# Kernel tuning notes

Hardware: AMD Instinct MI355X
Metric: run time of the kernel (lower is better)

## Reference

```python
import jax, jax.numpy as jnp
import numpy as np

B, S, D, H = 1, 1024, 1024, 16
DR, DV, R = 64, 64, 256          # rope head dim, v head dim, kv_lora_rank (qk_nope_head_dim = 0)
V, L, E, F, TOPK = 32000, 2, 4, 4096, 2
EPS, THETA, LB_WEIGHT = 1e-6, 10000.0, 0.01
SCALE = DR ** -0.5               # q_head_dim = nope(0) + rope(64)


def rms_norm(x, w):
    return x * jax.lax.rsqrt(jnp.mean(x * x, axis=-1, keepdims=True) + EPS) * w


def rotate_half(x):
    h = x.shape[-1] // 2
    return jnp.concatenate([-x[..., h:], x[..., :h]], axis=-1)


def apply_rope(x, cos, sin):
    # DeepSeek-V3 rotary: interleaved->half reorder, then rotate-half
    *lead, d = x.shape
    x = x.reshape(*lead, d // 2, 2).swapaxes(-1, -2).reshape(*lead, d)
    return x * cos + rotate_half(x) * sin


def setup_inputs() -> dict:
    key = jax.random.key(0)
    ks = iter(jax.random.split(key, 40))
    w = lambda shape: (0.02 * jax.random.normal(next(ks), shape)).astype(jnp.float32)
    return dict(
        tokens=jax.random.randint(next(ks), (B, S), 0, V, dtype=jnp.int32),
        embed=w((V, D)),                      # tied embedding / lm_head
        q_w=w((L, H * DR, D)),                # q_proj (q_lora_rank=None)
        kva_w=w((L, R + DR, D)),              # kv_a_proj_with_mqa
        kva_ln=jnp.ones((L, R), jnp.float32), # kv_a_layernorm (RMSNorm)
        kvb_w=w((L, H * DV, R)),              # kv_b_proj (nope=0 -> values only)
        o_w=w((L, D, H * DV)),
        norm1_w=jnp.ones((L, D), jnp.float32),
        norm2_w=jnp.ones((L, D), jnp.float32),
        router_w=w((L, E, D)),
        router_b=jnp.zeros((L, E), jnp.float32),
        w1=w((L, E, D, F)),
        b1=jnp.zeros((L, E, F), jnp.float32),
        w2=w((L, E, F, D)),
        b2=jnp.zeros((L, E, D), jnp.float32),
        final_norm_w=jnp.ones((D,), jnp.float32),
    )


def _layer(x, p, cos, sin, mask):
    # --- MLHA attention (DeepSeek-V3, qk_nope=0 => keys are shared rope k_pe) ---
    h = rms_norm(x, p['norm1_w'])
    q = (h @ p['q_w'].T).reshape(B, S, H, DR).transpose(0, 2, 1, 3)        # [B,H,S,DR]
    kva = h @ p['kva_w'].T                                                 # [B,S,R+DR]
    ckv, k_pe = kva[..., :R], kva[..., R:]
    v = (rms_norm(ckv, p['kva_ln']) @ p['kvb_w'].T).reshape(B, S, H, DV).transpose(0, 2, 1, 3)
    q = apply_rope(q, cos[None, None], sin[None, None])
    k = apply_rope(k_pe[:, None], cos[None, None], sin[None, None])[:, 0]  # [B,S,DR] shared across heads
    scores = jnp.einsum('bhsd,btd->bhst', q, k) * SCALE + mask
    attn = jax.nn.softmax(scores, axis=-1)
    o = jnp.einsum('bhst,bhtd->bhsd', attn, v).transpose(0, 2, 1, 3).reshape(B, S, H * DV)
    x = x + o @ p['o_w'].T
    # --- MoE FFN (top-k routing, renormalized gates, switch-style aux loss) ---
    h2 = rms_norm(x, p['norm2_w']).reshape(B * S, D)
    probs = jax.nn.softmax(h2 @ p['router_w'].T + p['router_b'], axis=-1)  # [T,E]
    topv, topi = jax.lax.top_k(probs, TOPK)
    gates = topv / jnp.sum(topv, axis=-1, keepdims=True)
    sel = jax.nn.one_hot(topi, E, dtype=probs.dtype)                       # [T,K,E]
    combine = jnp.einsum('tke,tk->te', sel, gates)                         # [T,E]
    hmid = jax.nn.gelu(jnp.einsum('td,edf->tef', h2, p['w1']) + p['b1'], approximate=False)
    y = jnp.einsum('tef,efd->ted', hmid, p['w2']) + p['b2']                # [T,E,D]
    ff = jnp.einsum('te,ted->td', combine, y).reshape(B, S, D)
    frac = jnp.mean(jnp.max(sel, axis=1), axis=0)                          # token fraction per expert
    aux = E * jnp.sum(frac * jnp.mean(probs, axis=0))
    return x + ff, aux


def reference(tokens, embed, q_w, kva_w, kva_ln, kvb_w, o_w, norm1_w, norm2_w,
              router_w, router_b, w1, b1, w2, b2, final_norm_w):
    x = embed[tokens]                                                      # [B,S,D]
    inv = 1.0 / (THETA ** (jnp.arange(0, DR, 2, dtype=jnp.float32) / DR))
    freqs = jnp.arange(S, dtype=jnp.float32)[:, None] * inv[None, :]
    emb = jnp.concatenate([freqs, freqs], axis=-1)
    cos, sin = jnp.cos(emb), jnp.sin(emb)                                  # [S,DR]
    mask = jnp.where(jnp.triu(jnp.ones((S, S), bool), 1), -jnp.inf, 0.0)[None, None]
    stacked = dict(q_w=q_w, kva_w=kva_w, kva_ln=kva_ln, kvb_w=kvb_w, o_w=o_w,
                   norm1_w=norm1_w, norm2_w=norm2_w, router_w=router_w, router_b=router_b,
                   w1=w1, b1=b1, w2=w2, b2=b2)

    def step(carry, p):
        x, aux = carry
        x, a = _layer(x, p, cos, sin, mask)
        return (x, aux + a), None

    (x, aux), _ = jax.lax.scan(step, (x, jnp.float32(0.0)), stacked)
    x = rms_norm(x, final_norm_w)
    logits = x @ embed.T                                                   # tied lm_head
    return logits, aux * LB_WEIGHT
```

## Files before the change

### kernel.cpp

```cpp
#include <hip/hip_runtime.h>
#include <hip/hip_bf16.h>
#include <math.h>

typedef __hip_bfloat16 bf16;
typedef __attribute__((ext_vector_type(8))) short short8;
typedef __attribute__((ext_vector_type(4))) short short4v;
typedef __attribute__((ext_vector_type(4))) float f32x4;

static constexpr int SEQ  = 1024;
static constexpr int DIM  = 1024;
static constexpr int NH   = 16;
static constexpr int DRR  = 64;
static constexpr int RR   = 256;
static constexpr int KVAN = RR + DRR;
static constexpr int VOC  = 32000;
static constexpr int NEXP = 4;
static constexpr int FFD  = 4096;
static constexpr int NSLOT = SEQ*2;
static constexpr float EPSF = 1e-6f;
static constexpr float ATT_SCALE = 0.125f;
static constexpr float LBW = 0.01f;

__device__ __forceinline__ bool is_bf(const uint32_t* mg){ return *mg == 0x3F803F80u; }
__device__ __forceinline__ float ldin(const void* p, size_t i, bool bf){
// ... 189 lines not shown
}

__global__ __launch_bounds__(256) void k_gather2(const float* __restrict__ h2,
    const int* __restrict__ tos, short* __restrict__ S){
  const int slot = blockIdx.x, tid = threadIdx.x;
  const int t = tos[slot];
  const int i = tid*4;
  const float4 v = *(const float4*)&h2[(size_t)t*DIM + i];
  const float vv[4] = {v.x, v.y, v.z, v.w};
  short4v h, l;
  #pragma unroll
  for (int q = 0; q < 4; ++q){ short a,b; split2(vv[q], a, b); h[q]=a; l[q]=b; }
  *(short4v*)&S[(size_t)slot*2*DIM + i] = h;
  *(short4v*)&S[(size_t)slot*2*DIM + DIM + i] = l;
}

__device__ __forceinline__ void tg_stage(const short* __restrict__ A, int lda, int ac,
    const short* __restrict__ B, int ldb, int bc, int bm, int bn,
    short* sA, short* sB, int wid, int rA, int ss){
  #pragma unroll
  for (int j = 0; j < 4; ++j){
    const int row = wid*32 + j*8 + rA;
    gload16(A + (size_t)(bm+row)*lda + ac + ss*8, sA + (wid*32 + j*8)*64);
    gload16(B + (size_t)(bn+row)*ldb + bc + ss*8, sB + (wid*32 + j*8)*64);
  }
}

#define TG_MFMAS(sAp, sBp)                                                      \
    _Pragma("unroll")                                                           \
    for (int kk = 0; kk < 2; ++kk){                                             \
      short8 a[4], b[4];                                                        \
      _Pragma("unroll")                                                         \
      for (int f = 0; f < 4; ++f){                                              \
        const int ar = wr*64 + f*16 + lr;                                       \
        a[f] = *(const short8*)&(sAp)[ar*64 + (((kk*4+lks)^(ar&7)))*8];         \
        const int br = wc*64 + f*16 + lr;                                       \
        b[f] = *(const short8*)&(sBp)[br*64 + (((kk*4+lks)^(br&7)))*8];         \
      }                                                                         \
      _Pragma("unroll")                                                         \
      for (int f = 0; f < 4; ++f)                                               \
        _Pragma("unroll")                                                       \
        for (int g = 0; g < 4; ++g)                                             \
          acc[f*4+g] = __builtin_amdgcn_mfma_f32_16x16x32_bf16(                 \
              a[f], b[g], acc[f*4+g], 0, 0, 0);                                 \
    }

#define TG_KADDR(st)                                                            \
  const int kt = (st)*64;                                                       \
  const int t = (kt >= 2*K) ? 2 : (kt >= K) ? 1 : 0;                            \
  const int ko = kt - t*K;                                                      \
  const int ac = ko + ((t == 2) ? K : 0);                                       \
  const int bc = ko + ((t == 1) ? K : 0);

template<int MODE>
__global__ __launch_bounds__(256) void k_tgemm_wt(
    const short* __restrict__ A, int lda,
    const short* __restrict__ W, int ldb, int K, int nt,
    float* __restrict__ C, int N, int S, float* __restrict__ Cpart){
  __shared__ alignas(16) short sA[128*64];
  __shared__ alignas(16) short sB[128*64];
  const int tid = threadIdx.x;
  const int wid = tid >> 6, lane = tid & 63;
  const int wr = wid >> 1, wc = wid & 1;
  const int bm = blockIdx.y * 128, bn = blockIdx.x * 128;
  const int rA = lane >> 3, ss = (lane & 7) ^ rA;
  const int lr = lane & 15, lks = lane >> 4;
  f32x4 acc[16];
  #pragma unroll
  for (int i = 0; i < 16; ++i) acc[i] = f32x4{0,0,0,0};

  const int nsteps = (nt*K) >> 6;
  const int per = (nsteps + S - 1)/S;
  const int st0 = blockIdx.z*per, st1 = min(nsteps, st0 + per);
  for (int st = st0; st < st1; ++st){
    TG_KADDR(st)
    tg_stage(A, lda, ac, W, ldb, bc, bm, bn, sA, sB, wid, rA, ss);
    __syncthreads();
    TG_MFMAS(sA, sB)
    __syncthreads();
  }
  const int r4 = lks*4, cj = lr;
  if (S == 1){
    #pragma unroll
    for (int f = 0; f < 4; ++f)
      #pragma unroll
      for (int g = 0; g < 4; ++g)
        #pragma unroll
        for (int r = 0; r < 4; ++r){
          const int gm = bm + wr*64 + f*16 + r4 + r;
          const int gn = bn + wc*64 + g*16 + cj;
          if (gn >= N) continue;
          const size_t idx = (size_t)gm*N + gn;
          if (MODE == 0) C[idx] = acc[f*4+g][r];
          else           C[idx] += acc[f*4+g][r];
        }
  } else {
    const int M = gridDim.y * 128;
    float* P = Cpart + (size_t)blockIdx.z*M*N;
    #pragma unroll
    for (int f = 0; f < 4; ++f)
      #pragma unroll
      for (int g = 0; g < 4; ++g)
        #pragma unroll
        for (int r = 0; r < 4; ++r){
          const int gm = bm + wr*64 + f*16 + r4 + r;
          const int gn = bn + wc*64 + g*16 + cj;
          if (gn >= N) continue;
          P[(size_t)gm*N + gn] = acc[f*4+g][r];
        }
  }
}

__global__ __launch_bounds__(512, 2) void k_tgemm_wtL(
    const short* __restrict__ A, int lda,
    const short* __restrict__ W, int ldb, int K,
    float* __restrict__ C, int N){
  __shared__ alignas(16) short sA[2][256*64];
  __shared__ alignas(16) short sB[2][256*64];
  const int tid = threadIdx.x;
  const int wid = tid >> 6, lane = tid & 63;
  const int wr = wid >> 2, wc = wid & 3;
  const int T = gridDim.x * gridDim.y;
  const int p = blockIdx.x + gridDim.x * blockIdx.y;
  const int xcd = p & 7, idx = p >> 3;
  const int q = T >> 3, r = T & 7;
  const int u = ((xcd < r) ? xcd*(q+1) : r*(q+1) + (xcd-r)*q) + idx;
  const int bn = (u >> 2) * 256;
  const int bm = (u & 3) * 256;
  const int rA = lane >> 3, ss = (lane & 7) ^ rA;
  const int lr = lane & 15, lks = lane >> 4;
  f32x4 acc[32];
  #pragma unroll
  for (int i = 0; i < 32; ++i) acc[i] = f32x4{0,0,0,0};

  auto stage = [&](int ko, int buf){
    #pragma unroll
    for (int j = 0; j < 4; ++j){
      const int row = wid*32 + j*8 + rA;
      gload16(A + (size_t)(bm+row)*lda + ko + ss*8, sA[buf] + (wid*32 + j*8)*64);
      gload16(W + (size_t)(bn+row)*ldb + ko + ss*8, sB[buf] + (wid*32 + j*8)*64);
    }
  };

  const int nsteps = K >> 6;
  stage(0, 0);
  asm volatile("s_waitcnt vmcnt(0)" ::: "memory");
  __builtin_amdgcn_s_barrier();
  int cur = 0;
  for (int st = 0; st < nsteps; ++st){
    const bool pf = (st + 1 < nsteps);
    if (pf) stage((st + 1)*64, cur^1);
    __builtin_amdgcn_s_setprio(1);
    #pragma unroll
    for (int kk = 0; kk < 2; ++kk){
      short8 a[8], b[4];
      #pragma unroll
      for (int f = 0; f < 8; ++f){
        const int ar = wr*128 + f*16 + lr;
        a[f] = *(const short8*)&sA[cur][ar*64 + (((kk*4+lks)^(ar&7)))*8];
      }
      #pragma unroll
      for (int g = 0; g < 4; ++g){
        const int br = wc*64 + g*16 + lr;
        b[g] = *(const short8*)&sB[cur][br*64 + (((kk*4+lks)^(br&7)))*8];
      }
      #pragma unroll
      for (int f = 0; f < 8; ++f)
        #pragma unroll
        for (int g = 0; g < 4; ++g)
          acc[f*4+g] = __builtin_amdgcn_mfma_f32_16x16x32_bf16(
              a[f], b[g], acc[f*4+g], 0, 0, 0);
    }
    __builtin_amdgcn_s_setprio(0);
    if (pf){
      asm volatile("s_waitcnt vmcnt(0)" ::: "memory");
      __builtin_amdgcn_s_barrier();
      cur ^= 1;
    }
  }
  const int r4 = lks*4, cj = lr;
  #pragma unroll
  for (int f = 0; f < 8; ++f)
    #pragma unroll
    for (int g = 0; g < 4; ++g)
      #pragma unroll
      for (int rr = 0; rr < 4; ++rr){
        const int gm = bm + wr*128 + f*16 + r4 + rr;
        const int gn = bn + wc*64 + g*16 + cj;
        if (gn >= N) continue;
        C[(size_t)gm*N + gn] = acc[f*4+g][rr];
      }
}

template<int MODE>
__global__ __launch_bounds__(256) void k_redw(const float* __restrict__ Cpart,
    float* __restrict__ C, int total, int S){
  const int i = blockIdx.x*256 + threadIdx.x;
  if (i >= total) return;
  float v = 0.f;
  for (int s = 0; s < S; ++s) v += Cpart[(size_t)s*total + i];
  if (MODE == 0) C[i] = v;
  else           C[i] += v;
}

template<int ACT, int OSPLIT>
__global__ __launch_bounds__(256) void k_tgemm_grp(
    const short* __restrict__ A, int lda,
    const short* __restrict__ Wall, int ldb, int K, int nt,
    const void* __restrict__ bias, size_t biofs, size_t perexp_bias,
    float* __restrict__ Cf, short* __restrict__ Cs,
    const int* __restrict__ meta, int N, const uint32_t* mg,
    int S, float* __restrict__ Cpart){
  __shared__ alignas(16) short sA[2][128*64];
  __shared__ alignas(16) short sB[2][128*64];
  const bool bf = is_bf(mg);
  const int e = blockIdx.z / S, zs = blockIdx.z - e*S;
  const int cnt = meta[e], off = meta[NEXP + e];
  const int r0 = blockIdx.y * 128;
  if (r0 >= cnt) return;
  const int rows_valid = min(128, cnt - r0);
  const int bm = off + r0, bn = blockIdx.x * 128;
  const short* W = Wall + (size_t)e*(size_t)N*ldb;
  const size_t bib = biofs + (size_t)e * perexp_bias;

  const int tid = threadIdx.x;
  const int wid = tid >> 6, lane = tid & 63;
  const int wr = wid >> 1, wc = wid & 1;
  const int rA = lane >> 3, ss = (lane & 7) ^ rA;
  const int lr = lane & 15, lks = lane >> 4;
  f32x4 acc[16];
  #pragma unroll
  for (int i = 0; i < 16; ++i) acc[i] = f32x4{0,0,0,0};

  const int nsteps = (nt*K) >> 6;
  const int per = (nsteps + S - 1)/S;
  const int st0 = zs*per, st1 = min(nsteps, st0 + per);
  {
    TG_KADDR(st0)
    tg_stage(A, lda, ac, W, ldb, bc, bm, bn, sA[0], sB[0], wid, rA, ss);
    asm volatile("s_waitcnt vmcnt(0)" ::: "memory");
    __builtin_amdgcn_s_barrier();
  }
  int cur = 0;
  for (int st = st0; st < st1; ++st){
    const bool pf = (st + 1 < st1);
    if (pf){
      TG_KADDR(st+1)
      tg_stage(A, lda, ac, W, ldb, bc, bm, bn, sA[cur^1], sB[cur^1], wid, rA, ss);
    }
    __builtin_amdgcn_s_setprio(1);
    TG_MFMAS(sA[cur], sB[cur])
    __builtin_amdgcn_s_setprio(0);
    if (pf){
      asm volatile("s_waitcnt vmcnt(0)" ::: "memory");
      __builtin_amdgcn_s_barrier();
      cur ^= 1;
    }
  }
  const int r4 = lks*4, cj = lr;
  if (S == 1){
    #pragma unroll
    for (int f = 0; f < 4; ++f)
      #pragma unroll
      for (int g = 0; g < 4; ++g)
        #pragma unroll
        for (int r = 0; r < 4; ++r){
          const int rin = wr*64 + f*16 + r4 + r;
          if (rin >= rows_valid) continue;
          const int gn = bn + wc*64 + g*16 + cj;
          float v = acc[f*4+g][r] + ldin(bias, bib + gn, bf);
          if (ACT == 1) v = 0.5f * v * (1.f + erff(v * 0.70710678118654752f));
          if (OSPLIT){
            short hi, lo; split2(v, hi, lo);
            const size_t idx = (size_t)(bm + rin)*2*N + gn;
            Cs[idx] = hi; Cs[idx + N] = lo;
          } else {
            Cf[(size_t)(bm + rin)*N + gn] = v;
          }
        }
  } else {
    float* P = Cpart + (size_t)zs*NSLOT*N;
    #pragma unroll
    for (int f = 0; f < 4; ++f)
      #pragma unroll
      for (int g = 0; g < 4; ++g)
        #pragma unroll
        for (int r = 0; r < 4; ++r){
          const int rin = wr*64 + f*16 + r4 + r;
          if (rin >= rows_valid) continue;
          const int gn = bn + wc*64 + g*16 + cj;
          P[(size_t)(bm + rin)*N + gn] = acc[f*4+g][r];
        }
  }
}

template<int ACT, int OSPLIT>
__global__ __launch_bounds__(512, 2) void k_tgemm_grpF(
    const short* __restrict__ A, int lda,
    const short* __restrict__ Wall, int ldb, int K,
    const void* __restrict__ bias, size_t biofs, size_t perexp_bias,
    float* __restrict__ Cf, short* __restrict__ Cs,
    const int* __restrict__ meta, int N, const uint32_t* mg,
    int S, float* __restrict__ Cpart){
  __shared__ alignas(16) short sAh[256*64];
  __shared__ alignas(16) short sAl[256*64];
  __shared__ alignas(16) short sBh[256*64];
  __shared__ alignas(16) short sBl[256*64];
  const bool bf = is_bf(mg);
  const int e = blockIdx.z / S, zs = blockIdx.z - e*S;
  const int cnt = meta[e], off = meta[NEXP + e];
  const int r0 = blockIdx.y * 256;
  if (r0 >= cnt) return;
  const int rows_valid = min(256, cnt - r0);
  const int bm = off + r0, bn = blockIdx.x * 256;
  const short* W = Wall + (size_t)e*(size_t)N*ldb;
  const size_t bib = biofs + (size_t)e * perexp_bias;

  const int tid = threadIdx.x;
  const int wid = tid >> 6, lane = tid & 63;
  const int wr = wid >> 2, wc = wid & 3;
  const int rA = lane >> 3, ss = (lane & 7) ^ rA;
  const int lr = lane & 15, lks = lane >> 4;
  f32x4 acc[32];
  #pragma unroll
  for (int i = 0; i < 32; ++i) acc[i] = f32x4{0,0,0,0};

  const int nsteps = K >> 6;
  const int per = (nsteps + S - 1)/S;
  const int st0 = zs*per, st1 = min(nsteps, st0 + per);
  for (int st = st0; st < st1; ++st){
    const int ko = st*64;
    #pragma unroll
    for (int j = 0; j < 4; ++j){
      const int row = wid*32 + j*8 + rA;
      const size_t arow = (size_t)(bm+row)*lda;
      const size_t brow = (size_t)(bn+row)*ldb;
      const int dst = (wid*32 + j*8)*64;
      gload16(A + arow + ko + ss*8,     sAh + dst);
      gload16(A + arow + K + ko + ss*8, sAl + dst);
      gload16(W + brow + ko + ss*8,     sBh + dst);
      gload16(W + brow + K + ko + ss*8, sBl + dst);
    }
    __syncthreads();
    __builtin_amdgcn_s_setprio(1);
    #pragma unroll
    for (int kk = 0; kk < 2; ++kk){
      short8 bh[4], bl[4];
      #pragma unroll
      for (int g = 0; g < 4; ++g){
        const int br = wc*64 + g*16 + lr;
        const int bo = br*64 + (((kk*4+lks)^(br&7)))*8;
        bh[g] = *(const short8*)&sBh[bo];
        bl[g] = *(const short8*)&sBl[bo];
      }
      #pragma unroll
      for (int f = 0; f < 8; ++f){
        const int ar = wr*128 + f*16 + lr;
        const int ao = ar*64 + (((kk*4+lks)^(ar&7)))*8;
        const short8 ah = *(const short8*)&sAh[ao];
        const short8 al = *(const short8*)&sAl[ao];
        #pragma unroll
        for (int g = 0; g < 4; ++g){
          acc[f*4+g] = __builtin_amdgcn_mfma_f32_16x16x32_bf16(ah, bh[g], acc[f*4+g], 0, 0, 0);
          acc[f*4+g] = __builtin_amdgcn_mfma_f32_16x16x32_bf16(ah, bl[g], acc[f*4+g], 0, 0, 0);
          acc[f*4+g] = __builtin_amdgcn_mfma_f32_16x16x32_bf16(al, bh[g], acc[f*4+g], 0, 0, 0);
        }
      }
    }
    __builtin_amdgcn_s_setprio(0);
    __syncthreads();
  }
  const int r4 = lks*4, cj = lr;
  if (S == 1){
    #pragma unroll
    for (int f = 0; f < 8; ++f)
      #pragma unroll
      for (int g = 0; g < 4; ++g)
        #pragma unroll
        for (int r = 0; r < 4; ++r){
          const int rin = wr*128 + f*16 + r4 + r;
          if (rin >= rows_valid) continue;
          const int gn = bn + wc*64 + g*16 + cj;
          float v = acc[f*4+g][r] + ldin(bias, bib + gn, bf);
          if (ACT == 1) v = 0.5f * v * (1.f + erff(v * 0.70710678118654752f));
          if (OSPLIT){
            short hi, lo; split2(v, hi, lo);
            const size_t idx = (size_t)(bm + rin)*2*N + gn;
            Cs[idx] = hi; Cs[idx + N] = lo;
          } else {
            Cf[(size_t)(bm + rin)*N + gn] = v;
          }
        }
  } else {
    float* P = Cpart + (size_t)zs*NSLOT*N;
    #pragma unroll
    for (int f = 0; f < 8; ++f)
      #pragma unroll
      for (int g = 0; g < 4; ++g)
        #pragma unroll
        for (int r = 0; r < 4; ++r){
          const int rin = wr*128 + f*16 + r4 + r;
          if (rin >= rows_valid) continue;
          const int gn = bn + wc*64 + g*16 + cj;
          P[(size_t)(bm + rin)*N + gn] = acc[f*4+g][r];
        }
  }
}

template<int ACT, int OSPLIT>
__global__ __launch_bounds__(256) void k_redg(const float* __restrict__ Cpart, int S,
    const int* __restrict__ eid,
    const void* __restrict__ bias, size_t biofs, size_t perexp_bias,
    float* __restrict__ Cf, short* __restrict__ Cs, int N, const uint32_t* mg){
  const bool bf = is_bf(mg);
  const int slot = blockIdx.x;
  const int e = eid[slot];
  const size_t bib = biofs + (size_t)e * perexp_bias;
  for (int n = threadIdx.x; n < N; n += 256){
    float v = 0.f;
    for (int s = 0; s < S; ++s)
      v += Cpart[(size_t)s*NSLOT*N + (size_t)slot*N + n];
    v += ldin(bias, bib + n, bf);
    if (ACT == 1) v = 0.5f * v * (1.f + erff(v * 0.70710678118654752f));
    if (OSPLIT){
      short hi, lo; split2(v, hi, lo);
      const size_t idx = (size_t)slot*2*N + n;
      Cs[idx] = hi; Cs[idx + N] = lo;
    } else {
      Cf[(size_t)slot*N + n] = v;
    }
  }
}

__global__ __launch_bounds__(512) void k_ropeq2(const float* __restrict__ qraw,
    const float* __restrict__ cosb, const float* __restrict__ sinb,
    short* __restrict__ Qsp){
  const int t = blockIdx.x, tid = threadIdx.x;
  const int hh = tid >> 5, i = tid & 31;
  const size_t base = (size_t)t*DIM + hh*DRR;
  const float u0 = qraw[base + 2*i];
  const float u1 = qraw[base + 2*i + 1];
  const float c = cosb[t*32 + i], s = sinb[t*32 + i];
  const float o0 = u0*c - u1*s;
  const float o1 = u1*c + u0*s;
  short h0,l0,h1,l1;
  split2(o0,h0,l0); split2(o1,h1,l1);
  short* q = Qsp + ((size_t)hh*SEQ + t)*128;
  q[i] = h0;      q[64+i] = l0;
  q[i+32] = h1;   q[96+i] = l1;
}

__global__ void k_ropek2(const float* __restrict__ kva,
    const float* __restrict__ cosb, const float* __restrict__ sinb,
    short* __restrict__ Kb){
  const int t = blockIdx.x, i = threadIdx.x;
  const float u0 = kva[(size_t)t*KVAN + RR + 2*i];
  const float u1 = kva[(size_t)t*KVAN + RR + 2*i + 1];
  const float c = cosb[t*32 + i], s = sinb[t*32 + i];
  const float o0 = u0*c - u1*s;
  const float o1 = u1*c + u0*s;
  short h0,l0,h1,l1;
  split2(o0,h0,l0); split2(o1,h1,l1);
  short* k = Kb + (size_t)t*128;
  k[i] = h0;      k[64+i] = l0;
  k[i+32] = h1;   k[96+i] = l1;
}

__global__ __launch_bounds__(256) void k_vsplit(const float* __restrict__ vbuf,
    short* __restrict__ Vt){
  __shared__ float tbuf[32][33];
  const int kv0 = blockIdx.x*32, d0 = blockIdx.y*32;
  const int c = threadIdx.x & 31, rb = threadIdx.x >> 5;
  #pragma unroll
  for (int p = 0; p < 4; ++p){
    const int r = rb + p*8;
    tbuf[r][c] = vbuf[(size_t)(kv0 + r)*DIM + d0 + c];
  }
  __syncthreads();
  #pragma unroll
  for (int p = 0; p < 4; ++p){
    const int rr = rb + p*8;
    const int dg = d0 + rr;
    const int h = dg >> 6, dl = dg & 63;
    short hi, lo; split2(tbuf[c][rr], hi, lo);
    const size_t o = ((size_t)h*64 + dl)*2048 + kv0 + c;
    Vt[o] = hi; Vt[o + 1024] = lo;
  }
}

__global__ __launch_bounds__(256) void k_fattn(
    const short* __restrict__ Qsp, const short* __restrict__ Kb,
    const short* __restrict__ Vt, float* __restrict__ outb){
  __shared__ alignas(16) short Qsh[64*64], Qsl[64*64];
  __shared__ alignas(16) short Ksh[64*64], Ksl[64*64];
  __shared__ alignas(16) short Vsh[64*64], Vsl[64*64];
  __shared__ alignas(16) short Ph[64*64], Pl[64*64];
  const int qt = blockIdx.x, hh = blockIdx.y;
  const int qbase = qt*64;
  const int tid = threadIdx.x;
  const int w = tid >> 6, lane = tid & 63;
  const int lr = lane & 15, lks = lane >> 4;
  const int r4 = lks*4, cj = lr;

  stage64(Qsp + ((size_t)hh*SEQ + qbase)*128,      128, Qsh, w, lane);
  stage64(Qsp + ((size_t)hh*SEQ + qbase)*128 + 64, 128, Qsl, w, lane);

  float m_r[4], l_r[4], alpha[4], rmax[4], rsum[4];
  f32x4 o[4];
  #pragma unroll
  for (int r = 0; r < 4; ++r){ m_r[r] = -3.0e38f; l_r[r] = 0.f; }
  #pragma unroll
  for (int g = 0; g < 4; ++g) o[g] = f32x4{0,0,0,0};
  __syncthreads();

  for (int kt = 0; kt <= qt; ++kt){
    const int kvbase = kt*64;
    stage64(Kb + (size_t)kvbase*128,        128, Ksh, w, lane);
    stage64(Kb + (size_t)kvbase*128 + 64,   128, Ksl, w, lane);
    stage64(Vt + (size_t)hh*64*2048 + kvbase,        2048, Vsh, w, lane);
    stage64(Vt + (size_t)hh*64*2048 + 1024 + kvbase, 2048, Vsl, w, lane);
    __syncthreads();

    f32x4 s[4];
    #pragma unroll
    for (int g = 0; g < 4; ++g) s[g] = f32x4{0,0,0,0};
    #pragma unroll
    for (int term = 0; term < 3; ++term){
      const short* Ab = (term == 2) ? Qsl : Qsh;
      const short* Bb = (term == 1) ? Ksl : Ksh;
      #pragma unroll
      for (int ks = 0; ks < 2; ++ks){
        const int arow = w*16 + lr;
        const short8 a = *(const short8*)&Ab[arow*64 + (((ks*4+lks)^(arow&7))*8)];
        #pragma unroll
        for (int g = 0; g < 4; ++g){
          const int brow = g*16 + lr;
          const short8 b = *(const short8*)&Bb[brow*64 + (((ks*4+lks)^(brow&7))*8)];
          s[g] = __builtin_amdgcn_mfma_f32_16x16x32_bf16(a, b, s[g], 0, 0, 0);
        }
      }
    }
    #pragma unroll
    for (int r = 0; r < 4; ++r) rmax[r] = -3.0e38f;
    #pragma unroll
    for (int g = 0; g < 4; ++g)
      #pragma unroll
      for (int r = 0; r < 4; ++r){
        float v = s[g][r] * ATT_SCALE;
        if (kvbase + g*16 + cj > qbase + w*16 + r4 + r) v = -3.0e38f;
        s[g][r] = v;
        rmax[r] = fmaxf(rmax[r], v);
      }
    #pragma unroll
    for (int msk = 1; msk < 16; msk <<= 1)
      #pragma unroll
      for (int r = 0; r < 4; ++r)
        rmax[r] = fmaxf(rmax[r], __shfl_xor(rmax[r], msk));
    #pragma unroll
    for (int r = 0; r < 4; ++r){
      const float mn = fmaxf(m_r[r], rmax[r]);
      alpha[r] = expf(m_r[r] - mn);
      m_r[r] = mn;
      rsum[r] = 0.f;
    }
    #pragma unroll
    for (int g = 0; g < 4; ++g)
      #pragma unroll
      for (int r = 0; r < 4; ++r){
        const float p = expf(s[g][r] - m_r[r]);
        s[g][r] = p;
        rsum[r] += p;
      }
    #pragma unroll
    for (int msk = 1; msk < 16; msk <<= 1)
      #pragma unroll
      for (int r = 0; r < 4; ++r)
        rsum[r] += __shfl_xor(rsum[r], msk);
    #pragma unroll
    for (int r = 0; r < 4; ++r)
      l_r[r] = l_r[r]*alpha[r] + rsum[r];
    #pragma unroll
    for (int g = 0; g < 4; ++g)
      #pragma unroll
      for (int r = 0; r < 4; ++r)
        o[g][r] *= alpha[r];
    #pragma unroll
    for (int g = 0; g < 4; ++g)
      #pragma unroll
      for (int r = 0; r < 4; ++r){
        short hi, lo; split2(s[g][r], hi, lo);
        const int prow = w*16 + r4 + r;
        const int sl = g*2 + (cj >> 3);
        const int addr = prow*64 + ((sl ^ (prow & 7))*8) + (cj & 7);
        Ph[addr] = hi; Pl[addr] = lo;
      }
    #pragma unroll
    for (int term = 0; term < 3; ++term){
      const short* Ab = (term == 2) ? Pl : Ph;
      const short* Bb = (term == 1) ? Vsl : Vsh;
      #pragma unroll
      for (int ks = 0; ks < 2; ++ks){
        const int arow = w*16 + lr;
        const short8 a = *(const short8*)&Ab[arow*64 + (((ks*4+lks)^(arow&7))*8)];
        #pragma unroll
        for (int g = 0; g < 4; ++g){
          const int brow = g*16 + lr;
          const short8 b = *(const short8*)&Bb[brow*64 + (((ks*4+lks)^(brow&7))*8)];
          o[g] = __builtin_amdgcn_mfma_f32_16x16x32_bf16(a, b, o[g], 0, 0, 0);
        }
      }
    }
    __syncthreads();
  }
  #pragma unroll
  for (int g = 0; g < 4; ++g)
    #pragma unroll
    for (int r = 0; r < 4; ++r)
      outb[(size_t)(qbase + w*16 + r4 + r)*DIM + hh*64 + g*16 + cj] = o[g][r] / l_r[r];
}

template<int MODE>
__global__ __launch_bounds__(256) void k_mgemm_wt(const float* __restrict__ A,
    const void* __restrict__ W, size_t wofs, float* __restrict__ C,
    int M, int N, int K, const uint32_t* mg){
  __shared__ alignas(16) short As[64][40];
  __shared__ alignas(16) short Bs[64][40];
  const bool bf = is_bf(mg);
  const int tid = threadIdx.x;
  const int bm = blockIdx.x * 64, bn = blockIdx.y * 64;
  const int wid = tid >> 6, lane = tid & 63;
  const int wr = wid >> 1, wc = wid & 1;
  const int lrow = lane & 15, lk = (lane >> 4) * 8;
  const int srow = tid >> 3, sk = (tid & 7) * 4;
  f32x4 acc00{0,0,0,0}, acc01{0,0,0,0}, acc10{0,0,0,0}, acc11{0,0,0,0};
  for (int kt = 0; kt < K; kt += 32){
    #pragma unroll
    for (int p = 0; p < 2; ++p){
      const int r = srow + p*32;
      const size_t abase = (size_t)(bm + r)*K + kt + sk;
      As[r][sk+0] = f2bs(A[abase+0]);
      As[r][sk+1] = f2bs(A[abase+1]);
      As[r][sk+2] = f2bs(A[abase+2]);
      As[r][sk+3] = f2bs(A[abase+3]);
      const size_t wbase = wofs + (size_t)(bn + r)*K + kt + sk;
      Bs[r][sk+0] = f2bs(ldin(W, wbase+0, bf));
      Bs[r][sk+1] = f2bs(ldin(W, wbase+1, bf));
      Bs[r][sk+2] = f2bs(ldin(W, wbase+2, bf));
      Bs[r][sk+3] = f2bs(ldin(W, wbase+3, bf));
    }
    __syncthreads();
    const short8 a0 = *(const short8*)&As[wr*32 +      lrow][lk];
    const short8 a1 = *(const short8*)&As[wr*32 + 16 + lrow][lk];
    const short8 b0 = *(const short8*)&Bs[wc*32 +      lrow][lk];
    const short8 b1 = *(const short8*)&Bs[wc*32 + 16 + lrow][lk];
    acc00 = __builtin_amdgcn_mfma_f32_16x16x32_bf16(a0, b0, acc00, 0, 0, 0);
    acc01 = __builtin_amdgcn_mfma_f32_16x16x32_bf16(a0, b1, acc01, 0, 0, 0);
    acc10 = __builtin_amdgcn_mfma_f32_16x16x32_bf16(a1, b0, acc10, 0, 0, 0);
    acc11 = __builtin_amdgcn_mfma_f32_16x16x32_bf16(a1, b1, acc11, 0, 0, 0);
    __syncthreads();
  }
  const int r4 = (lane >> 4) * 4, cj = lane & 15;
  #pragma unroll
  for (int fm = 0; fm < 2; ++fm)
    #pragma unroll
    for (int fn = 0; fn < 2; ++fn){
      const f32x4 av = fm == 0 ? (fn == 0 ? acc00 : acc01) : (fn == 0 ? acc10 : acc11);
      #pragma unroll
      for (int r = 0; r < 4; ++r){
        const int gm = bm + wr*32 + fm*16 + r4 + r;
        const int gn = bn + wc*32 + fn*16 + cj;
        const size_t idx = (size_t)gm*N + gn;
        if (MODE == 0) C[idx] = av[r];
        else           C[idx] += av[r];
// ... 399 lines not shown
```

Before: 1.421 ms.

## Double-buffer LDS tiles in grouped expert GEMM with K-step 32 prefetch

The grouped MoE GEMM now splits its LDS tiles into two buffers of half the K depth (32 instead of 64). The next K-slice is prefetched with async global-to-LDS loads while MFMAs run on the current buffer, and one barrier per step replaces two. The aim is to hide global load latency behind compute, at the cost of twice as many loop iterations and barriers per K and a new XOR swizzle over 4 chunks instead of 8.

```diff
diff --git a/kernel.cpp b/kernel.cpp
--- a/kernel.cpp
+++ b/kernel.cpp
@@ -515,10 +515,10 @@
     float* __restrict__ Cf, short* __restrict__ Cs,
     const int* __restrict__ meta, int N, const uint32_t* mg,
     int S, float* __restrict__ Cpart){
-  __shared__ alignas(16) short sAh[256*64];
-  __shared__ alignas(16) short sAl[256*64];
-  __shared__ alignas(16) short sBh[256*64];
-  __shared__ alignas(16) short sBl[256*64];
+  __shared__ alignas(16) short sAh[2][256*32];
+  __shared__ alignas(16) short sAl[2][256*32];
+  __shared__ alignas(16) short sBh[2][256*32];
+  __shared__ alignas(16) short sBl[2][256*32];
   const bool bf = is_bf(mg);
   const int e = blockIdx.z / S, zs = blockIdx.z - e*S;
   const int cnt = meta[e], off = meta[NEXP + e];
@@ -532,46 +532,53 @@
   const int tid = threadIdx.x;
   const int wid = tid >> 6, lane = tid & 63;
   const int wr = wid >> 2, wc = wid & 3;
-  const int rA = lane >> 3, ss = (lane & 7) ^ rA;
+  const int rA4 = lane >> 2, ss4 = (lane & 3) ^ (rA4 & 3);
   const int lr = lane & 15, lks = lane >> 4;
   f32x4 acc[32];
   #pragma unroll
   for (int i = 0; i < 32; ++i) acc[i] = f32x4{0,0,0,0};
 
-  const int nsteps = K >> 6;
+  auto stage = [&](int ko, int buf){
+    #pragma unroll
+    for (int j = 0; j < 2; ++j){
+      const int row = j*128 + wid*16 + rA4;
+      const int dst = (j*128 + wid*16)*32 + lane*8;
+      const size_t arow = (size_t)(bm+row)*lda;
+      const size_t brow = (size_t)(bn+row)*ldb;
+      const int sc = ko + ss4*8;
+      gload16(A + arow + sc,     &sAh[buf][dst]);
+      gload16(A + arow + K + sc, &sAl[buf][dst]);
+      gload16(W + brow + sc,     &sBh[buf][dst]);
+      gload16(W + brow + K + sc, &sBl[buf][dst]);
+    }
+  };
+
+  const int nsteps = K >> 5;
   const int per = (nsteps + S - 1)/S;
   const int st0 = zs*per, st1 = min(nsteps, st0 + per);
+  stage(st0*32, 0);
+  asm volatile("s_waitcnt vmcnt(0)" ::: "memory");
+  __builtin_amdgcn_s_barrier();
+  int cur = 0;
   for (int st = st0; st < st1; ++st){
-    const int ko = st*64;
-    #pragma unroll
-    for (int j = 0; j < 4; ++j){
-      const int row = wid*32 + j*8 + rA;
-      const size_t arow = (size_t)(bm+row)*lda;
-      const size_t brow = (size_t)(bn+row)*ldb;
-      const int dst = (wid*32 + j*8)*64;
-      gload16(A + arow + ko + ss*8,     sAh + dst);
-      gload16(A + arow + K + ko + ss*8, sAl + dst);
-      gload16(W + brow + ko + ss*8,     sBh + dst);
-      gload16(W + brow + K + ko + ss*8, sBl + dst);
-    }
-    __syncthreads();
+    const bool pf = (st + 1 < st1);
+    if (pf) stage((st + 1)*32, cur^1);
     __builtin_amdgcn_s_setprio(1);
-    #pragma unroll
-    for (int kk = 0; kk < 2; ++kk){
+    {
       short8 bh[4], bl[4];
       #pragma unroll
       for (int g = 0; g < 4; ++g){
         const int br = wc*64 + g*16 + lr;
-        const int bo = br*64 + (((kk*4+lks)^(br&7)))*8;
-        bh[g] = *(const short8*)&sBh[bo];
-        bl[g] = *(const short8*)&sBl[bo];
+        const int bo = br*32 + ((lks ^ (br&3))*8);
+        bh[g] = *(const short8*)&sBh[cur][bo];
+        bl[g] = *(const short8*)&sBl[cur][bo];
       }
       #pragma unroll
       for (int f = 0; f < 8; ++f){
         const int ar = wr*128 + f*16 + lr;
-        const int ao = ar*64 + (((kk*4+lks)^(ar&7)))*8;
-        const short8 ah = *(const short8*)&sAh[ao];
-        const short8 al = *(const short8*)&sAl[ao];
+        const int ao = ar*32 + ((lks ^ (ar&3))*8);
+        const short8 ah = *(const short8*)&sAh[cur][ao];
+        const short8 al = *(const short8*)&sAl[cur][ao];
         #pragma unroll
         for (int g = 0; g < 4; ++g){
           acc[f*4+g] = __builtin_amdgcn_mfma_f32_16x16x32_bf16(ah, bh[g], acc[f*4+g], 0, 0, 0);
@@ -581,7 +588,11 @@
       }
     }
     __builtin_amdgcn_s_setprio(0);
-    __syncthreads();
+    if (pf){
+      asm volatile("s_waitcnt vmcnt(0)" ::: "memory");
+      __builtin_amdgcn_s_barrier();
+      cur ^= 1;
+    }
   }
   const int r4 = lks*4, cj = lr;
   if (S == 1){
```

New measurement: 1.420 ms. About the same (-0.0%).
